# Performance work log

Hardware: AMD Instinct MI355X
Metric: run time of the kernel (lower is better)

## Reference

```python
import jax, jax.numpy as jnp
import numpy as np
from jax import lax

NUM_HEADS = 8
DIM = 192
EPS = 1e-12  # torch F.normalize eps


def setup_inputs() -> dict:
    key = jax.random.key(0)
    k1, k2, k3, k4 = jax.random.split(key, 4)
    b, c, h, w = 8, DIM, 128, 128
    x = jax.random.normal(k1, (b, c, h, w), dtype=jnp.float32)
    # 1x1 qkv conv weight stored as [3c, c]; depthwise 3x3 weight [3c,1,3,3]; proj 1x1 [c,c]
    w_qkv = jax.random.normal(k2, (3 * c, c), dtype=jnp.float32) * (1.0 / np.sqrt(c))
    w_dw = jax.random.normal(k3, (3 * c, 1, 3, 3), dtype=jnp.float32) * (1.0 / 3.0)
    w_proj = jax.random.normal(k4, (c, c), dtype=jnp.float32) * (1.0 / np.sqrt(c))
    temperature = jnp.ones((NUM_HEADS, 1, 1), dtype=jnp.float32)
    return {"x": x, "w_qkv": w_qkv, "w_dw": w_dw, "w_proj": w_proj, "temperature": temperature}


def _l2_normalize(t):
    # matches torch.nn.functional.normalize(dim=-1, eps=1e-12)
    n = jnp.sqrt(jnp.sum(t * t, axis=-1, keepdims=True))
    return t / jnp.maximum(n, EPS)


def reference(x, w_qkv, w_dw, w_proj, temperature):
    b, c, h, w = x.shape
    heads = NUM_HEADS
    cd = c // heads  # per-head channel dim
    # 1x1 qkv conv (no bias) as einsum
    qkv = jnp.einsum('bchw,oc->bohw', x, w_qkv)  # [b, 3c, h, w]
    # depthwise 3x3 conv, groups = 3c
    qkv = lax.conv_general_dilated(
        qkv, w_dw, window_strides=(1, 1), padding='SAME',
        feature_group_count=3 * c,
        dimension_numbers=('NCHW', 'OIHW', 'NCHW'))
    q, k, v = jnp.split(qkv, 3, axis=1)  # each [b, c, h, w]
    hw = h * w
    q = q.reshape(b, heads, cd, hw)
    k = k.reshape(b, heads, cd, hw)
    v = v.reshape(b, heads, cd, hw)
    q = _l2_normalize(q)
    k = _l2_normalize(k)
    # channel-wise attention: [b, heads, cd, cd]
    attn = jnp.einsum('bhcn,bhdn->bhcd', q, k) * temperature[None]
    attn = jax.nn.softmax(attn, axis=-1)
    out = jnp.einsum('bhcd,bhdn->bhcn', attn, v)  # [b, heads, cd, hw]
    out = out.reshape(b, c, h, w)
    out = jnp.einsum('bchw,oc->bohw', out, w_proj)
    return out
```

## Files before the change

### kernel.cpp

```cpp
#include <hip/hip_runtime.h>

#define HW 16384
#define CC 192
#define C3 576
#define NB 8
#define NH 8

typedef __attribute__((ext_vector_type(8))) short bfrag;
typedef __attribute__((ext_vector_type(4))) float f32x4;
typedef __attribute__((ext_vector_type(4))) unsigned short us4;

#define MFMA16(a, b, c) __builtin_amdgcn_mfma_f32_16x16x32_bf16(a, b, c, 0, 0, 0)

typedef __attribute__((address_space(3))) unsigned int lds_u32;
typedef __attribute__((address_space(1))) unsigned int glb_u32;
__device__ __forceinline__ void gl_lds16(const void* g, void* l) {
  __builtin_amdgcn_global_load_lds((const glb_u32*)g, (lds_u32*)l, 16, 0, 0);
}

__device__ __forceinline__ unsigned short f2bf(float f) {
  unsigned int u = __float_as_uint(f);
  u += 0x7fffu + ((u >> 16) & 1u);
  return (unsigned short)(u >> 16);
}
__device__ __forceinline__ float bf2f(unsigned short s) {
  return __uint_as_float(((unsigned int)s) << 16);
}
__device__ __forceinline__ float bf2f_s(short s) {
  return __uint_as_float(((unsigned int)(unsigned short)s) << 16);
}

#define OFF_XT   0ull
#define SZ_XT    ((size_t)NB * HW * CC * 2)
#define OFF_WQ   (OFF_XT + SZ_XT)
#define SZ_WQ    ((size_t)C3 * CC * 2)
#define OFF_QKV  (OFF_WQ + SZ_WQ)
#define SZ_QKV   ((size_t)NB * C3 * HW * 2)
#define OFF_QKVD (OFF_QKV + SZ_QKV)
#define SZ_QKVD  ((size_t)NB * C3 * HW * 2)
#define OFF_S    (OFF_QKVD + SZ_QKVD)
#define SZ_S     ((size_t)NB * NH * 32 * 32 * 4)
#define OFF_SSQ  (OFF_S + SZ_S)
#define SZ_SSQ   ((size_t)NB * 384 * 4)
#define OFF_M    (OFF_SSQ + SZ_SSQ)
#define SZ_M     ((size_t)NB * CC * CC * 2)

__global__ __launch_bounds__(256) void k_xt(const float* __restrict__ x,
                                            unsigned short* __restrict__ xt) {
  __shared__ unsigned short tile[64 * 72];
  const int pb = blockIdx.x * 64;
  const int cb = blockIdx.y * 64;
  const int b  = blockIdx.z;
  const int t  = threadIdx.x;
  {
    const int cl = t >> 2, pl = (t & 3) * 16;
    const float* src = x + ((size_t)b * CC + cb + cl) * HW + pb + pl;
    bfrag v0, v1;
#pragma unroll
    for (int q4 = 0; q4 < 2; ++q4) {
      float4 f = *reinterpret_cast<const float4*>(src + q4 * 4);
      v0[q4 * 4 + 0] = (short)f2bf(f.x); v0[q4 * 4 + 1] = (short)f2bf(f.y);
      v0[q4 * 4 + 2] = (short)f2bf(f.z); v0[q4 * 4 + 3] = (short)f2bf(f.w);
    }
#pragma unroll
    for (int q4 = 0; q4 < 2; ++q4) {
      float4 f = *reinterpret_cast<const float4*>(src + 8 + q4 * 4);
      v1[q4 * 4 + 0] = (short)f2bf(f.x); v1[q4 * 4 + 1] = (short)f2bf(f.y);
      v1[q4 * 4 + 2] = (short)f2bf(f.z); v1[q4 * 4 + 3] = (short)f2bf(f.w);
    }
    *reinterpret_cast<bfrag*>(&tile[cl * 72 + pl]) = v0;
    *reinterpret_cast<bfrag*>(&tile[cl * 72 + pl + 8]) = v1;
  }
  __syncthreads();
  {
    const int pl = t >> 2, cl = (t & 3) * 16;
    bfrag o0, o1;
#pragma unroll
    for (int e = 0; e < 8; ++e) o0[e] = (short)tile[(cl + e) * 72 + pl];
#pragma unroll
    for (int e = 0; e < 8; ++e) o1[e] = (short)tile[(cl + 8 + e) * 72 + pl];
    unsigned short* dst = xt + ((size_t)b * HW + pb + pl) * CC + cb + cl;
    *reinterpret_cast<bfrag*>(dst) = o0;
    *reinterpret_cast<bfrag*>(dst + 8) = o1;
  }
}

__global__ __launch_bounds__(256) void k_wpack(const float* __restrict__ w,
                                               unsigned short* __restrict__ wp) {
  const int g = blockIdx.x * 256 + threadIdx.x;
  if (g >= 216 * 64) return;
  const int frag = g >> 6, lane = g & 63;
  const int mb = frag / 24, r = frag % 24, s = r >> 2, i = r & 3;
  const int row = mb * 64 + i * 16 + (lane & 15);
  const int col = s * 32 + (lane >> 4) * 8;
  const float* src = w + (size_t)row * CC + col;
  float4 f0 = *reinterpret_cast<const float4*>(src);
  float4 f1 = *reinterpret_cast<const float4*>(src + 4);
  us4 o0, o1;
  o0[0] = f2bf(f0.x); o0[1] = f2bf(f0.y); o0[2] = f2bf(f0.z); o0[3] = f2bf(f0.w);
  o1[0] = f2bf(f1.x); o1[1] = f2bf(f1.y); o1[2] = f2bf(f1.z); o1[3] = f2bf(f1.w);
  *reinterpret_cast<us4*>(wp + (size_t)g * 8) = o0;
  *reinterpret_cast<us4*>(wp + (size_t)g * 8 + 4) = o1;
}

__global__ __launch_bounds__(256, 3) void k_gemm_qkv(const unsigned short* __restrict__ Wp,
                                                     const unsigned short* __restrict__ Xt,
                                                     unsigned short* __restrict__ Y) {
  __shared__ __attribute__((aligned(16))) char sB[49152];
  const int nb = blockIdx.x;
  const int b  = blockIdx.y;
  const int tid = threadIdx.x;
  const int wave = tid >> 6, lane = tid & 63;
  const int lrow = lane & 15, lk = (lane >> 4) * 8, lr4 = (lane >> 4) * 4;

  const char* Bc = (const char*)(Xt + ((size_t)b * HW + (size_t)nb * 128) * CC);
#pragma unroll
  for (int t = 0; t < 12; ++t) {
    const int L = wave * 12288 + t * 1024 + lane * 16;
    const int row = L / 384;
    const int rem = L - row * 384;
    gl_lds16(Bc + row * 384 + (rem ^ ((row & 7) << 4)), sB + wave * 12288 + t * 1024);
  }
  asm volatile("s_waitcnt vmcnt(0)" ::: "memory");
  __syncthreads();

  const int swz = (lrow & 7) << 4;
  const int base0 = (wave * 32 + lrow) * 384;
  const f32x4 z4 = {0.f, 0.f, 0.f, 0.f};

#pragma unroll 1
  for (int mb = 0; mb < 9; ++mb) {
    const unsigned short* Wb = Wp + (size_t)mb * 24 * 512;
    bfrag af[6][4];
#pragma unroll
    for (int s = 0; s < 6; ++s)
#pragma unroll
      for (int i = 0; i < 4; ++i)
        af[s][i] = *reinterpret_cast<const bfrag*>(Wb + ((s * 4 + i) * 64 + lane) * 8);

    f32x4 acc[4][2];
#pragma unroll
    for (int i = 0; i < 4; ++i) { acc[i][0] = z4; acc[i][1] = z4; }
#pragma unroll
    for (int s = 0; s < 6; ++s) {
      const int kbs = ((s * 32 + lk) * 2) ^ swz;
      bfrag b0 = *reinterpret_cast<const bfrag*>(sB + base0 + kbs);
      bfrag b1 = *reinterpret_cast<const bfrag*>(sB + base0 + 16 * 384 + kbs);
#pragma unroll
      for (int i = 0; i < 4; ++i) {
        acc[i][0] = MFMA16(b0, af[s][i], acc[i][0]);
        acc[i][1] = MFMA16(b1, af[s][i], acc[i][1]);
      }
    }
    unsigned short* Yb = Y + ((size_t)b * C3 + mb * 64) * HW + nb * 128 + wave * 32;
#pragma unroll
    for (int i = 0; i < 4; ++i) {
      unsigned short* rp = Yb + (size_t)(i * 16 + lrow) * HW;
#pragma unroll
      for (int j = 0; j < 2; ++j) {
        uint2 pk;
        pk.x = (unsigned int)f2bf(acc[i][j][0]) | ((unsigned int)f2bf(acc[i][j][1]) << 16);
        pk.y = (unsigned int)f2bf(acc[i][j][2]) | ((unsigned int)f2bf(acc[i][j][3]) << 16);
        *reinterpret_cast<uint2*>(rp + j * 16 + lr4) = pk;
      }
    }
  }
}

__global__ __launch_bounds__(256) void k_dwconv(const unsigned short* __restrict__ in,
                                                const float* __restrict__ wd,
                                                unsigned short* __restrict__ outb) {
  const int strip = blockIdx.x;
  const int ch = blockIdx.y;
  const int b = blockIdx.z;
  const int t = threadIdx.x;
  const unsigned short* ip = in + ((size_t)b * C3 + ch) * HW;
  const float* w = wd + ch * 9;
  const int p = strip * 2048 + t * 8;
  const int y = p >> 7, x0 = p & 127;
  float acc[8] = {0.f, 0.f, 0.f, 0.f, 0.f, 0.f, 0.f, 0.f};
#pragma unroll
  for (int dy = 0; dy < 3; ++dy) {
    int yy = y + dy - 1;
    if (yy < 0 || yy > 127) continue;
    const unsigned short* row = ip + yy * 128;
    bfrag v = *reinterpret_cast<const bfrag*>(row + x0);
    float c[8];
#pragma unroll
    for (int e = 0; e < 8; ++e) c[e] = bf2f_s(v[e]);
    float left  = (x0 > 0)   ? bf2f(row[x0 - 1]) : 0.f;
    float right = (x0 < 120) ? bf2f(row[x0 + 8]) : 0.f;
    float wl = w[dy * 3 + 0], wc = w[dy * 3 + 1], wr = w[dy * 3 + 2];
    acc[0] += wl * left + wc * c[0] + wr * c[1];
#pragma unroll
    for (int e = 1; e < 7; ++e) acc[e] += wl * c[e - 1] + wc * c[e] + wr * c[e + 1];
    acc[7] += wl * c[6] + wc * c[7] + wr * right;
  }
  unsigned short* op = outb + ((size_t)b * C3 + ch) * HW + p;
  bfrag o;
#pragma unroll
  for (int e = 0; e < 8; ++e) o[e] = (short)f2bf(acc[e]);
  *reinterpret_cast<bfrag*>(op) = o;
}

__global__ __launch_bounds__(256) void k_vt(const unsigned short* __restrict__ Vd,
                                            unsigned short* __restrict__ VTo) {
  __shared__ unsigned short tile[64 * 72];
  const int pb = blockIdx.x * 64, cb = blockIdx.y * 64, b = blockIdx.z;
  const int t = threadIdx.x;
  {
    const int cl = t >> 2, ps = (t & 3) * 16;
    const unsigned short* src = Vd + ((size_t)b * C3 + 384 + cb + cl) * HW + pb + ps;
    bfrag v0 = *reinterpret_cast<const bfrag*>(src);
    bfrag v1 = *reinterpret_cast<const bfrag*>(src + 8);
    *reinterpret_cast<bfrag*>(&tile[cl * 72 + ps]) = v0;
    *reinterpret_cast<bfrag*>(&tile[cl * 72 + ps + 8]) = v1;
  }
  __syncthreads();
  {
    const int pl = t >> 2, cs = (t & 3) * 16;
    bfrag o0, o1;
#pragma unroll
    for (int e = 0; e < 8; ++e) o0[e] = (short)tile[(cs + e) * 72 + pl];
#pragma unroll
    for (int e = 0; e < 8; ++e) o1[e] = (short)tile[(cs + 8 + e) * 72 + pl];
    unsigned short* dst = VTo + ((size_t)b * HW + pb + pl) * CC + cb + cs;
    *reinterpret_cast<bfrag*>(dst) = o0;
    *reinterpret_cast<bfrag*>(dst + 8) = o1;
  }
}

__global__ __launch_bounds__(256) void k_gram(const unsigned short* __restrict__ Qd,
                                              float* __restrict__ S,
                                              float* __restrict__ ssq) {
  const int chunk = blockIdx.x;
  const int h = blockIdx.y, b = blockIdx.z;
  const int tid = threadIdx.x, wave = tid >> 6, lane = tid & 63;
  const int lrow = lane & 15, lk8 = (lane >> 4) * 8;
  const unsigned short* qb = Qd + ((size_t)b * C3 + h * 24) * HW;
  const unsigned short* kb = qb + (size_t)192 * HW;
  const int p0 = chunk * 1024 + wave * 256;
  f32x4 acc[2][2];
  const f32x4 z4 = {0.f, 0.f, 0.f, 0.f};
#pragma unroll
  for (int i = 0; i < 2; ++i)
#pragma unroll
    for (int j = 0; j < 2; ++j) acc[i][j] = z4;
  float sq[2] = {0.f, 0.f}, sk[2] = {0.f, 0.f};
  for (int s = 0; s < 8; ++s) {
    const int pp = p0 + s * 32 + lk8;
    bfrag aq[2], bk[2];
#pragma unroll
    for (int i = 0; i < 2; ++i) {
      aq[i] = *reinterpret_cast<const bfrag*>(qb + (size_t)(i * 16 + lrow) * HW + pp);
      bk[i] = *reinterpret_cast<const bfrag*>(kb + (size_t)(i * 16 + lrow) * HW + pp);
    }
#pragma unroll
    for (int i = 0; i < 2; ++i) {
#pragma unroll
      for (int e = 0; e < 8; ++e) {
        float qv = bf2f_s(aq[i][e]); sq[i] += qv * qv;
        float kv = bf2f_s(bk[i][e]); sk[i] += kv * kv;
      }
    }
#pragma unroll
    for (int i = 0; i < 2; ++i)
#pragma unroll
      for (int j = 0; j < 2; ++j) acc[i][j] = MFMA16(aq[i], bk[j], acc[i][j]);
  }
  float* Sb = S + (size_t)(b * 8 + h) * 1024;
  const int lr4 = (lane >> 4) * 4;
#pragma unroll
  for (int i = 0; i < 2; ++i)
#pragma unroll
    for (int j = 0; j < 2; ++j)
#pragma unroll
      for (int r = 0; r < 4; ++r)
        atomicAdd(&Sb[(i * 16 + lr4 + r) * 32 + j * 16 + lrow], acc[i][j][r]);
#pragma unroll
  for (int i = 0; i < 2; ++i) {
    float v = sq[i];
    v += __shfl_xor(v, 16); v += __shfl_xor(v, 32);
    float wv = sk[i];
    wv += __shfl_xor(wv, 16); wv += __shfl_xor(wv, 32);
    const int c = i * 16 + lrow;
    if ((lane >> 4) == 0 && c < 24) {
      atomicAdd(&ssq[b * 384 + h * 24 + c], v);
      atomicAdd(&ssq[b * 384 + 192 + h * 24 + c], wv);
    }
  }
}

__global__ __launch_bounds__(64) void k_attn(const float* __restrict__ S,
                                             const float* __restrict__ ssq,
                                             const float* __restrict__ wproj,
                                             const float* __restrict__ temp,
                                             unsigned short* __restrict__ Mp) {
  const int h = blockIdx.x, b = blockIdx.y;
  __shared__ float A[24][25];
  __shared__ float nq[24], nk[24];
  const float* Sb = S + (size_t)(b * 8 + h) * 1024;
  const float* sq = ssq + b * 384 + h * 24;
  const float* sk = ssq + b * 384 + 192 + h * 24;
  const int t = threadIdx.x;
  if (t < 24) {
    nq[t] = fmaxf(sqrtf(sq[t]), 1e-12f);
    nk[t] = fmaxf(sqrtf(sk[t]), 1e-12f);
  }
  __syncthreads();
  if (t < 24) {
    const float tp = temp[h];
    float row[24];
    float mx = -1e30f;
#pragma unroll
    for (int d = 0; d < 24; ++d) {
      row[d] = Sb[t * 32 + d] / (nq[t] * nk[d]) * tp;
      mx = fmaxf(mx, row[d]);
    }
    float s = 0.f;
#pragma unroll
    for (int d = 0; d < 24; ++d) { row[d] = __expf(row[d] - mx); s += row[d]; }
    const float inv = 1.f / s;
#pragma unroll
    for (int d = 0; d < 24; ++d) A[t][d] = row[d] * inv;
  }
  __syncthreads();
  for (int idx = t; idx < 192 * 24; idx += 64) {
    const int o = idx / 24, dd = idx % 24;
    const float* wrow = wproj + o * 192 + h * 24;
    float a = 0.f;
#pragma unroll
    for (int cc = 0; cc < 24; ++cc) a += wrow[cc] * A[cc][dd];
    const int c = h * 24 + dd;
    const int mb = o >> 6, i = (o >> 4) & 3, lr = o & 15;
    const int s = c >> 5, hi = (c >> 3) & 3, e = c & 7;
    const int off = ((mb * 24 + s * 4 + i) * 64 + hi * 16 + lr) * 8 + e;
    Mp[(size_t)b * CC * CC + off] = f2bf(a);
  }
}

__global__ __launch_bounds__(256, 3) void k_gemm_out(const unsigned short* __restrict__ Mp,
                                                     const unsigned short* __restrict__ VT,
                                                     float* __restrict__ out) {
  __shared__ __attribute__((aligned(16))) char sB[49152];
  const int nb = blockIdx.x;
  const int b  = blockIdx.y;
  const int tid = threadIdx.x;
  const int wave = tid >> 6, lane = tid & 63;
  const int lrow = lane & 15, lk = (lane >> 4) * 8, lr4 = (lane >> 4) * 4;

  const char* Bc = (const char*)(VT + ((size_t)b * HW + (size_t)nb * 128) * CC);
#pragma unroll
  for (int t = 0; t < 12; ++t) {
    const int L = wave * 12288 + t * 1024 + lane * 16;
    const int row = L / 384;
    const int rem = L - row * 384;
    gl_lds16(Bc + row * 384 + (rem ^ ((row & 7) << 4)), sB + wave * 12288 + t * 1024);
  }
  asm volatile("s_waitcnt vmcnt(0)" ::: "memory");
  __syncthreads();

  const int swz = (lrow & 7) << 4;
  const int base0 = (wave * 32 + lrow) * 384;
  const f32x4 z4 = {0.f, 0.f, 0.f, 0.f};

#pragma unroll 1
  for (int mb = 0; mb < 3; ++mb) {
    const unsigned short* Mb = Mp + (size_t)b * CC * CC + (size_t)mb * 24 * 512;
    bfrag af[6][4];
#pragma unroll
    for (int s = 0; s < 6; ++s)
#pragma unroll
      for (int i = 0; i < 4; ++i)
        af[s][i] = *reinterpret_cast<const bfrag*>(Mb + ((s * 4 + i) * 64 + lane) * 8);

    f32x4 acc[4][2];
#pragma unroll
    for (int i = 0; i < 4; ++i) { acc[i][0] = z4; acc[i][1] = z4; }
#pragma unroll
    for (int s = 0; s < 6; ++s) {
      const int kbs = ((s * 32 + lk) * 2) ^ swz;
      bfrag b0 = *reinterpret_cast<const bfrag*>(sB + base0 + kbs);
      bfrag b1 = *reinterpret_cast<const bfrag*>(sB + base0 + 16 * 384 + kbs);
#pragma unroll
      for (int i = 0; i < 4; ++i) {
        acc[i][0] = MFMA16(b0, af[s][i], acc[i][0]);
        acc[i][1] = MFMA16(b1, af[s][i], acc[i][1]);
      }
    }
    float* Ob = out + ((size_t)b * CC + mb * 64) * HW + nb * 128 + wave * 32;
#pragma unroll
    for (int i = 0; i < 4; ++i) {
      float* rp = Ob + (size_t)(i * 16 + lrow) * HW;
#pragma unroll
      for (int j = 0; j < 2; ++j)
        *reinterpret_cast<f32x4*>(rp + j * 16 + lr4) = acc[i][j];
    }
  }
}

extern "C" void kernel_launch(void* const* d_in, const int* in_sizes, int n_in,
                              void* d_out, int out_size, void* d_ws, size_t ws_size,
                              hipStream_t stream) {
  const float* x      = (const float*)d_in[0];
  const float* w_qkv  = (const float*)d_in[1];
  const float* w_dw   = (const float*)d_in[2];
  const float* w_proj = (const float*)d_in[3];
  const float* temp   = (const float*)d_in[4];
  float* out = (float*)d_out;
  char* ws = (char*)d_ws;

  unsigned short* XT   = (unsigned short*)(ws + OFF_XT);
  unsigned short* VT   = (unsigned short*)(ws + OFF_XT);
  unsigned short* WP   = (unsigned short*)(ws + OFF_WQ);
  unsigned short* QKV  = (unsigned short*)(ws + OFF_QKV);
  unsigned short* QKVD = (unsigned short*)(ws + OFF_QKVD);
  float* S   = (float*)(ws + OFF_S);
  float* SSQ = (float*)(ws + OFF_SSQ);
  unsigned short* MP  = (unsigned short*)(ws + OFF_M);

  hipMemsetAsync(ws + OFF_S, 0, SZ_S + SZ_SSQ, stream);
  k_wpack<<<54, 256, 0, stream>>>(w_qkv, WP);
  k_xt<<<dim3(HW / 64, CC / 64, NB), 256, 0, stream>>>(x, XT);
  k_gemm_qkv<<<dim3(HW / 128, NB), 256, 0, stream>>>(WP, XT, QKV);
  k_dwconv<<<dim3(8, C3, NB), 256, 0, stream>>>(QKV, w_dw, QKVD);
  k_vt<<<dim3(HW / 64, 3, NB), 256, 0, stream>>>(QKVD, VT);
  k_gram<<<dim3(16, NH, NB), 256, 0, stream>>>(QKVD, S, SSQ);
  k_attn<<<dim3(NH, NB), 64, 0, stream>>>(S, SSQ, w_proj, temp, MP);
  k_gemm_out<<<dim3(HW / 128, NB), 256, 0, stream>>>(MP, VT, out);
}
```

Before: 336.4 us.

## Fuse depthwise conv into Gram and V-transpose kernels, drop QKVD buffer

Removes the standalone depthwise-conv kernel and its full bf16 QKVD intermediate. Q/K depthwise conv is now computed inside the Gram kernel, which stages results in LDS for MFMA and accumulates squared norms. V depthwise conv is fused into the transpose kernel. This avoids writing and rereading a large intermediate, but the Gram kernel has only 512 blocks doing serial conv work, so occupancy and latency hiding may suffer.

```diff
diff --git a/kernel.cpp b/kernel.cpp
--- a/kernel.cpp
+++ b/kernel.cpp
@@ -36,9 +36,7 @@
 #define SZ_WQ    ((size_t)C3 * CC * 2)
 #define OFF_QKV  (OFF_WQ + SZ_WQ)
 #define SZ_QKV   ((size_t)NB * C3 * HW * 2)
-#define OFF_QKVD (OFF_QKV + SZ_QKV)
-#define SZ_QKVD  ((size_t)NB * C3 * HW * 2)
-#define OFF_S    (OFF_QKVD + SZ_QKVD)
+#define OFF_S    (OFF_QKV + SZ_QKV)
 #define SZ_S     ((size_t)NB * NH * 32 * 32 * 4)
 #define OFF_SSQ  (OFF_S + SZ_S)
 #define SZ_SSQ   ((size_t)NB * 384 * 4)
@@ -167,54 +165,156 @@
   }
 }
 
-__global__ __launch_bounds__(256) void k_dwconv(const unsigned short* __restrict__ in,
-                                                const float* __restrict__ wd,
-                                                unsigned short* __restrict__ outb) {
-  const int strip = blockIdx.x;
-  const int ch = blockIdx.y;
-  const int b = blockIdx.z;
-  const int t = threadIdx.x;
-  const unsigned short* ip = in + ((size_t)b * C3 + ch) * HW;
-  const float* w = wd + ch * 9;
-  const int p = strip * 2048 + t * 8;
-  const int y = p >> 7, x0 = p & 127;
-  float acc[8] = {0.f, 0.f, 0.f, 0.f, 0.f, 0.f, 0.f, 0.f};
-#pragma unroll
-  for (int dy = 0; dy < 3; ++dy) {
-    int yy = y + dy - 1;
-    if (yy < 0 || yy > 127) continue;
-    const unsigned short* row = ip + yy * 128;
-    bfrag v = *reinterpret_cast<const bfrag*>(row + x0);
-    float c[8];
-#pragma unroll
-    for (int e = 0; e < 8; ++e) c[e] = bf2f_s(v[e]);
-    float left  = (x0 > 0)   ? bf2f(row[x0 - 1]) : 0.f;
-    float right = (x0 < 120) ? bf2f(row[x0 + 8]) : 0.f;
-    float wl = w[dy * 3 + 0], wc = w[dy * 3 + 1], wr = w[dy * 3 + 2];
-    acc[0] += wl * left + wc * c[0] + wr * c[1];
-#pragma unroll
-    for (int e = 1; e < 7; ++e) acc[e] += wl * c[e - 1] + wc * c[e] + wr * c[e + 1];
-    acc[7] += wl * c[6] + wc * c[7] + wr * right;
-  }
-  unsigned short* op = outb + ((size_t)b * C3 + ch) * HW + p;
-  bfrag o;
-#pragma unroll
-  for (int e = 0; e < 8; ++e) o[e] = (short)f2bf(acc[e]);
-  *reinterpret_cast<bfrag*>(op) = o;
-}
-
-__global__ __launch_bounds__(256) void k_vt(const unsigned short* __restrict__ Vd,
-                                            unsigned short* __restrict__ VTo) {
+__global__ __launch_bounds__(256, 2) void k_dwgram(const unsigned short* __restrict__ QKV,
+                                                   const float* __restrict__ wd,
+                                                   float* __restrict__ S,
+                                                   float* __restrict__ ssq) {
+  __shared__ short lds[56 * 520];
+  const int strip = blockIdx.x, h = blockIdx.y, b = blockIdx.z;
+  const int tid = threadIdx.x, wave = tid >> 6, lane = tid & 63;
+  const int lrow = lane & 15, lk8 = (lane >> 4) * 8, lr4 = (lane >> 4) * 4;
+  const size_t qbase = ((size_t)b * C3 + h * 24) * HW;
+  const size_t kbase = qbase + (size_t)192 * HW;
+
+  const int p = lane * 8;
+  const int x0 = p & 127;
+
+  float sqp[6] = {0.f, 0.f, 0.f, 0.f, 0.f, 0.f};
+  float skp[6] = {0.f, 0.f, 0.f, 0.f, 0.f, 0.f};
+  f32x4 acc[2][2];
+  const f32x4 z4 = {0.f, 0.f, 0.f, 0.f};
+#pragma unroll
+  for (int i = 0; i < 2; ++i) { acc[i][0] = z4; acc[i][1] = z4; }
+
+  auto dwconv8 = [&](const unsigned short* ip, const float* w, int y, float* facc) {
+#pragma unroll
+    for (int e = 0; e < 8; ++e) facc[e] = 0.f;
+#pragma unroll
+    for (int dy = 0; dy < 3; ++dy) {
+      int yy = y + dy - 1;
+      if (yy < 0 || yy > 127) continue;
+      const unsigned short* row = ip + yy * 128;
+      bfrag v = *reinterpret_cast<const bfrag*>(row + x0);
+      float c[8];
+#pragma unroll
+      for (int e = 0; e < 8; ++e) c[e] = bf2f_s(v[e]);
+      float left  = (x0 > 0)   ? bf2f(row[x0 - 1]) : 0.f;
+      float right = (x0 < 120) ? bf2f(row[x0 + 8]) : 0.f;
+      float wl = w[dy * 3 + 0], wc = w[dy * 3 + 1], wr = w[dy * 3 + 2];
+      facc[0] += wl * left + wc * c[0] + wr * c[1];
+#pragma unroll
+      for (int e = 1; e < 7; ++e) facc[e] += wl * c[e - 1] + wc * c[e] + wr * c[e + 1];
+      facc[7] += wl * c[6] + wc * c[7] + wr * right;
+    }
+  };
+
+#pragma unroll 1
+  for (int chunk = 0; chunk < 4; ++chunk) {
+    const int y = strip * 16 + chunk * 4 + (p >> 7);
+#pragma unroll 1
+    for (int j = 0; j < 6; ++j) {
+      const int c = wave + 4 * j;
+      float facc[8];
+      dwconv8(QKV + qbase + (size_t)c * HW, wd + (h * 24 + c) * 9, y, facc);
+      {
+        float ss = 0.f;
+        bfrag o;
+#pragma unroll
+        for (int e = 0; e < 8; ++e) { ss += facc[e] * facc[e]; o[e] = (short)f2bf(facc[e]); }
+        sqp[j] += ss;
+        *reinterpret_cast<bfrag*>(&lds[c * 520 + p]) = o;
+      }
+      dwconv8(QKV + kbase + (size_t)c * HW, wd + (192 + h * 24 + c) * 9, y, facc);
+      {
+        float ss = 0.f;
+        bfrag o;
+#pragma unroll
+        for (int e = 0; e < 8; ++e) { ss += facc[e] * facc[e]; o[e] = (short)f2bf(facc[e]); }
+        skp[j] += ss;
+        *reinterpret_cast<bfrag*>(&lds[(24 + c) * 520 + p]) = o;
+      }
+    }
+    __syncthreads();
+#pragma unroll
+    for (int ks = 0; ks < 4; ++ks) {
+      const int pp = wave * 128 + ks * 32 + lk8;
+      bfrag aq[2], bk[2];
+#pragma unroll
+      for (int i = 0; i < 2; ++i) {
+        aq[i] = *reinterpret_cast<const bfrag*>(&lds[(i * 16 + lrow) * 520 + pp]);
+        bk[i] = *reinterpret_cast<const bfrag*>(&lds[(24 + i * 16 + lrow) * 520 + pp]);
+      }
+#pragma unroll
+      for (int i = 0; i < 2; ++i)
+#pragma unroll
+        for (int j2 = 0; j2 < 2; ++j2) acc[i][j2] = MFMA16(aq[i], bk[j2], acc[i][j2]);
+    }
+    __syncthreads();
+  }
+
+  float* Sb = S + (size_t)(b * 8 + h) * 1024;
+#pragma unroll
+  for (int i = 0; i < 2; ++i)
+#pragma unroll
+    for (int j2 = 0; j2 < 2; ++j2)
+#pragma unroll
+      for (int r = 0; r < 4; ++r)
+        atomicAdd(&Sb[(i * 16 + lr4 + r) * 32 + j2 * 16 + lrow], acc[i][j2][r]);
+
+#pragma unroll
+  for (int j = 0; j < 6; ++j) {
+    float v = sqp[j];
+    float wv = skp[j];
+#pragma unroll
+    for (int o = 1; o < 64; o <<= 1) { v += __shfl_xor(v, o); wv += __shfl_xor(wv, o); }
+    if (lane == 0) {
+      const int c = wave + 4 * j;
+      atomicAdd(&ssq[b * 384 + h * 24 + c], v);
+      atomicAdd(&ssq[b * 384 + 192 + h * 24 + c], wv);
+    }
+  }
+}
+
+__global__ __launch_bounds__(256) void k_dwvt(const unsigned short* __restrict__ QKV,
+                                              const float* __restrict__ wd,
+                                              unsigned short* __restrict__ VTo) {
   __shared__ unsigned short tile[64 * 72];
   const int pb = blockIdx.x * 64, cb = blockIdx.y * 64, b = blockIdx.z;
   const int t = threadIdx.x;
+  const int y = pb >> 7;
+  const int xs = pb & 127;
   {
     const int cl = t >> 2, ps = (t & 3) * 16;
-    const unsigned short* src = Vd + ((size_t)b * C3 + 384 + cb + cl) * HW + pb + ps;
-    bfrag v0 = *reinterpret_cast<const bfrag*>(src);
-    bfrag v1 = *reinterpret_cast<const bfrag*>(src + 8);
-    *reinterpret_cast<bfrag*>(&tile[cl * 72 + ps]) = v0;
-    *reinterpret_cast<bfrag*>(&tile[cl * 72 + ps + 8]) = v1;
+    const int gc = 384 + cb + cl;
+    const unsigned short* ip = QKV + ((size_t)b * C3 + gc) * HW;
+    const float* w = wd + gc * 9;
+    const int x0 = xs + ps;
+    float acc[16];
+#pragma unroll
+    for (int e = 0; e < 16; ++e) acc[e] = 0.f;
+#pragma unroll
+    for (int dy = 0; dy < 3; ++dy) {
+      int yy = y + dy - 1;
+      if (yy < 0 || yy > 127) continue;
+      const unsigned short* row = ip + yy * 128;
+      bfrag v0 = *reinterpret_cast<const bfrag*>(row + x0);
+      bfrag v1 = *reinterpret_cast<const bfrag*>(row + x0 + 8);
+      float c[16];
+#pragma unroll
+      for (int e = 0; e < 8; ++e) { c[e] = bf2f_s(v0[e]); c[8 + e] = bf2f_s(v1[e]); }
+      float left  = (x0 > 0)   ? bf2f(row[x0 - 1])  : 0.f;
+      float right = (x0 < 112) ? bf2f(row[x0 + 16]) : 0.f;
+      float wl = w[dy * 3 + 0], wc = w[dy * 3 + 1], wr = w[dy * 3 + 2];
+      acc[0] += wl * left + wc * c[0] + wr * c[1];
+#pragma unroll
+      for (int e = 1; e < 15; ++e) acc[e] += wl * c[e - 1] + wc * c[e] + wr * c[e + 1];
+      acc[15] += wl * c[14] + wc * c[15] + wr * right;
+    }
+    bfrag o0, o1;
+#pragma unroll
+    for (int e = 0; e < 8; ++e) { o0[e] = (short)f2bf(acc[e]); o1[e] = (short)f2bf(acc[8 + e]); }
+    *reinterpret_cast<bfrag*>(&tile[cl * 72 + ps]) = o0;
+    *reinterpret_cast<bfrag*>(&tile[cl * 72 + ps + 8]) = o1;
   }
   __syncthreads();
   {
@@ -227,67 +327,6 @@
     unsigned short* dst = VTo + ((size_t)b * HW + pb + pl) * CC + cb + cs;
     *reinterpret_cast<bfrag*>(dst) = o0;
     *reinterpret_cast<bfrag*>(dst + 8) = o1;
-  }
-}
-
-__global__ __launch_bounds__(256) void k_gram(const unsigned short* __restrict__ Qd,
-                                              float* __restrict__ S,
-                                              float* __restrict__ ssq) {
-  const int chunk = blockIdx.x;
-  const int h = blockIdx.y, b = blockIdx.z;
-  const int tid = threadIdx.x, wave = tid >> 6, lane = tid & 63;
-  const int lrow = lane & 15, lk8 = (lane >> 4) * 8;
-  const unsigned short* qb = Qd + ((size_t)b * C3 + h * 24) * HW;
-  const unsigned short* kb = qb + (size_t)192 * HW;
-  const int p0 = chunk * 1024 + wave * 256;
-  f32x4 acc[2][2];
-  const f32x4 z4 = {0.f, 0.f, 0.f, 0.f};
-#pragma unroll
-  for (int i = 0; i < 2; ++i)
-#pragma unroll
-    for (int j = 0; j < 2; ++j) acc[i][j] = z4;
-  float sq[2] = {0.f, 0.f}, sk[2] = {0.f, 0.f};
-  for (int s = 0; s < 8; ++s) {
-    const int pp = p0 + s * 32 + lk8;
-    bfrag aq[2], bk[2];
-#pragma unroll
-    for (int i = 0; i < 2; ++i) {
-      aq[i] = *reinterpret_cast<const bfrag*>(qb + (size_t)(i * 16 + lrow) * HW + pp);
-      bk[i] = *reinterpret_cast<const bfrag*>(kb + (size_t)(i * 16 + lrow) * HW + pp);
-    }
-#pragma unroll
-    for (int i = 0; i < 2; ++i) {
-#pragma unroll
-      for (int e = 0; e < 8; ++e) {
-        float qv = bf2f_s(aq[i][e]); sq[i] += qv * qv;
-        float kv = bf2f_s(bk[i][e]); sk[i] += kv * kv;
-      }
-    }
-#pragma unroll
-    for (int i = 0; i < 2; ++i)
-#pragma unroll
-      for (int j = 0; j < 2; ++j) acc[i][j] = MFMA16(aq[i], bk[j], acc[i][j]);
-  }
-  float* Sb = S + (size_t)(b * 8 + h) * 1024;
-  const int lr4 = (lane >> 4) * 4;
-#pragma unroll
-  for (int i = 0; i < 2; ++i)
-#pragma unroll
-    for (int j = 0; j < 2; ++j)
-#pragma unroll
-      for (int r = 0; r < 4; ++r)
-        atomicAdd(&Sb[(i * 16 + lr4 + r) * 32 + j * 16 + lrow], acc[i][j][r]);
-#pragma unroll
-  for (int i = 0; i < 2; ++i) {
-    float v = sq[i];
-    v += __shfl_xor(v, 16); v += __shfl_xor(v, 32);
-    float wv = sk[i];
-    wv += __shfl_xor(wv, 16); wv += __shfl_xor(wv, 32);
-    const int c = i * 16 + lrow;
-    if ((lane >> 4) == 0 && c < 24) {
-      atomicAdd(&ssq[b * 384 + h * 24 + c], v);
-      atomicAdd(&ssq[b * 384 + 192 + h * 24 + c], wv);
-    }
   }
 }
 
@@ -414,7 +453,6 @@
   unsigned short* VT   = (unsigned short*)(ws + OFF_XT);
   unsigned short* WP   = (unsigned short*)(ws + OFF_WQ);
   unsigned short* QKV  = (unsigned short*)(ws + OFF_QKV);
-  unsigned short* QKVD = (unsigned short*)(ws + OFF_QKVD);
   float* S   = (float*)(ws + OFF_S);
   float* SSQ = (float*)(ws + OFF_SSQ);
   unsigned short* MP  = (unsigned short*)(ws + OFF_M);
@@ -423,9 +461,8 @@
   k_wpack<<<54, 256, 0, stream>>>(w_qkv, WP);
   k_xt<<<dim3(HW / 64, CC / 64, NB), 256, 0, stream>>>(x, XT);
   k_gemm_qkv<<<dim3(HW / 128, NB), 256, 0, stream>>>(WP, XT, QKV);
-  k_dwconv<<<dim3(8, C3, NB), 256, 0, stream>>>(QKV, w_dw, QKVD);
-  k_vt<<<dim3(HW / 64, 3, NB), 256, 0, stream>>>(QKVD, VT);
-  k_gram<<<dim3(16, NH, NB), 256, 0, stream>>>(QKVD, S, SSQ);
+  k_dwgram<<<dim3(8, NH, NB), 256, 0, stream>>>(QKV, w_dw, S, SSQ);
+  k_dwvt<<<dim3(HW / 64, 3, NB), 256, 0, stream>>>(QKV, w_dw, VT);
   k_attn<<<dim3(NH, NB), 64, 0, stream>>>(S, SSQ, w_proj, temp, MP);
   k_gemm_out<<<dim3(HW / 128, NB), 256, 0, stream>>>(MP, VT, out);
 }
```

New measurement: 344.2 us. +2.3%, slower.
